# Kernel tuning notes

Measured on AMD Instinct MI355X. Metric: run time of the kernel, lower is better.

Reference implementation:

```python
import jax, jax.numpy as jnp
import numpy as np

N_NODES = 20000
N_EDGES = 640000
IN_NODE = 128
IN_EDGE = 16
HIDDEN = 64
OUT = 128
HEADS = 4
N_GRAPHS = 64
NEG_SLOPE = 0.2


def _glorot(key, shape):
    fan_in, fan_out = shape[0], shape[-1]
    s = jnp.sqrt(6.0 / (fan_in + fan_out)).astype(jnp.float32)
    return jax.random.uniform(key, shape, jnp.float32, -s, s)


def setup_inputs() -> dict:
    key = jax.random.key(0)
    ks = jax.random.split(key, 32)
    inp = {
        "x": jax.random.normal(ks[0], (N_NODES, IN_NODE), jnp.float32),
        "edge_attr": jax.random.normal(ks[1], (N_EDGES, IN_EDGE), jnp.float32),
        "edge_index": jax.random.randint(ks[2], (2, N_EDGES), 0, N_NODES),
        "batch": jnp.sort(jax.random.randint(ks[3], (N_NODES,), 0, N_GRAPHS)),
    }
    # layer dims: (in, out_per_head, concat)
    dims = [(IN_NODE, HIDDEN, True), (HIDDEN * HEADS, HIDDEN, True), (HIDDEN * HEADS, OUT, False)]
    k = 4
    for i, (cin, cout, concat) in enumerate(dims):
        hc = HEADS * cout
        inp[f"Wl{i}"] = _glorot(ks[k], (cin, hc)); k += 1
        inp[f"bl{i}"] = jnp.zeros((hc,), jnp.float32)
        inp[f"Wr{i}"] = _glorot(ks[k], (cin, hc)); k += 1
        inp[f"br{i}"] = jnp.zeros((hc,), jnp.float32)
        inp[f"We{i}"] = _glorot(ks[k], (IN_EDGE, hc)); k += 1
        inp[f"att{i}"] = _glorot(ks[k], (HEADS, cout)); k += 1
        inp[f"bias{i}"] = jnp.zeros((hc if concat else cout,), jnp.float32)
    return inp


def _gatv2_layer(x, edge_index, edge_attr, Wl, bl, Wr, br, We, att, bias, concat):
    """One PyG-style GATv2Conv layer with edge features."""
    H, C = att.shape
    N = x.shape[0]
    src, dst = edge_index[0], edge_index[1]
    xl = (x @ Wl + bl).reshape(N, H, C)  # messages from source
    xr = (x @ Wr + br).reshape(N, H, C)  # target query
    e = (edge_attr @ We).reshape(-1, H, C)
    m = jax.nn.leaky_relu(xl[src] + xr[dst] + e, NEG_SLOPE)  # [E,H,C]
    logits = jnp.einsum("ehc,hc->eh", m, att)  # [E,H]
    # scatter-softmax over edges grouped by destination node
    lmax = jax.ops.segment_max(logits, dst, num_segments=N)
    p = jnp.exp(logits - lmax[dst])
    denom = jax.ops.segment_sum(p, dst, num_segments=N)
    alpha = p / (denom[dst] + 1e-16)  # [E,H]
    out = jax.ops.segment_sum(alpha[:, :, None] * xl[src], dst, num_segments=N)  # [N,H,C]
    if concat:
        return out.reshape(N, H * C) + bias
    return out.mean(axis=1) + bias


def reference(x, edge_attr, edge_index, batch,
              Wl0, bl0, Wr0, br0, We0, att0, bias0,
              Wl1, bl1, Wr1, br1, We1, att1, bias1,
              Wl2, bl2, Wr2, br2, We2, att2, bias2):
    layers = [
        (Wl0, bl0, Wr0, br0, We0, att0, bias0, True),
        (Wl1, bl1, Wr1, br1, We1, att1, bias1, True),
        (Wl2, bl2, Wr2, br2, We2, att2, bias2, False),
    ]
    h = x
    for (Wl, bl, Wr, br, We, att, b, concat) in layers:
        h = _gatv2_layer(h, edge_index, edge_attr, Wl, bl, Wr, br, We, att, b, concat)
    # global max + mean pooling per graph
    x_max = jax.ops.segment_max(h, batch, num_segments=N_GRAPHS)
    s = jax.ops.segment_sum(h, batch, num_segments=N_GRAPHS)
    cnt = jax.ops.segment_sum(jnp.ones((h.shape[0], 1), h.dtype), batch, num_segments=N_GRAPHS)
    x_mean = s / jnp.maximum(cnt, 1.0)
    return jnp.concatenate([x_max, x_mean], axis=1)  # [G, 2*OUT]
```

## Files before the change

### kernel.cpp

```cpp
#include <hip/hip_runtime.h>

#define NB 8

typedef float f32x2 __attribute__((ext_vector_type(2)));

template <int K, int M>
__global__ __launch_bounds__(256) void node_gemm(
    const float* __restrict__ X, const float* __restrict__ W,
    const float* __restrict__ bias, float* __restrict__ Y) {
  constexpr int NPB = 16;
  constexpr int COLS4 = M / 4;
  constexpr int NG = 256 / COLS4;
  constexpr int RPN = NPB / NG;
  __shared__ float xs[NPB * K];
  const int tid = threadIdx.x;
  const int n0 = blockIdx.x * NPB;
  {
    const float4* X4 = reinterpret_cast<const float4*>(X + (size_t)n0 * K);
    float4* xs4 = reinterpret_cast<float4*>(xs);
    for (int i = tid; i < NPB * K / 4; i += 256) xs4[i] = X4[i];
  }
  __syncthreads();
  const int c4 = (tid % COLS4) * 4;
  const int r0 = (tid / COLS4) * RPN;
  float acc[RPN][4];
#pragma unroll
  for (int r = 0; r < RPN; ++r)
#pragma unroll
    for (int q = 0; q < 4; ++q) acc[r][q] = 0.f;

  for (int k = 0; k < K; k += 4) {
    float xv[RPN][4];
#pragma unroll
    for (int r = 0; r < RPN; ++r)
      *reinterpret_cast<float4*>(xv[r]) =
          *reinterpret_cast<const float4*>(&xs[(r0 + r) * K + k]);
#pragma unroll
    for (int j = 0; j < 4; ++j) {
      float wv[4];
      *reinterpret_cast<float4*>(wv) =
          *reinterpret_cast<const float4*>(&W[(size_t)(k + j) * M + c4]);
#pragma unroll
      for (int r = 0; r < RPN; ++r)
#pragma unroll
        for (int q = 0; q < 4; ++q)
          acc[r][q] = fmaf(xv[r][j], wv[q], acc[r][q]);
    }
  }
  float bv[4];
  *reinterpret_cast<float4*>(bv) = *reinterpret_cast<const float4*>(&bias[c4]);
#pragma unroll
  for (int r = 0; r < RPN; ++r) {
    float o[4];
#pragma unroll
    for (int q = 0; q < 4; ++q) o[q] = acc[r][q] + bv[q];
    *reinterpret_cast<float4*>(&Y[(size_t)(n0 + r0 + r) * M + c4]) =
        *reinterpret_cast<float4*>(o);
  }
}

__global__ void hist_b(const int* __restrict__ ei, int* __restrict__ kcnt,
                       int E, int bdiv) {
  int i = blockIdx.x * blockDim.x + threadIdx.x;
  if (i < E) atomicAdd(&kcnt[ei[E + i] * NB + ei[i] / bdiv], 1);
}

__global__ __launch_bounds__(1024) void blk_scan(
    const int* __restrict__ in, int* __restrict__ out1, int* __restrict__ bsum, int n) {
  __shared__ int buf[1024];
  const int tid = threadIdx.x;
  const int gid = blockIdx.x * 1024 + tid;
  int v = (gid < n) ? in[gid] : 0;
  buf[tid] = v;
  __syncthreads();
  for (int off = 1; off < 1024; off <<= 1) {
    int t = (tid >= off) ? buf[tid - off] : 0;
    __syncthreads();
    buf[tid] += t;
    __syncthreads();
  }
  if (gid < n) out1[gid] = buf[tid];
  if (tid == 1023) bsum[blockIdx.x] = buf[1023];
}

__global__ __launch_bounds__(256) void scan_bsum(int* __restrict__ bsum, int nb) {
  __shared__ int buf[256];
  const int tid = threadIdx.x;
  int v = (tid < nb) ? bsum[tid] : 0;
  buf[tid] = v;
  __syncthreads();
  for (int off = 1; off < 256; off <<= 1) {
    int t = (tid >= off) ? buf[tid - off] : 0;
    __syncthreads();
    buf[tid] += t;
    __syncthreads();
  }
  if (tid < nb) bsum[tid] = buf[tid];
}

__global__ void add_off(int* __restrict__ kptr, const int* __restrict__ bsum, int n) {
  int gid = blockIdx.x * blockDim.x + threadIdx.x;
  if (gid == 0) kptr[0] = 0;
  if (gid < n) {
    int blk = gid >> 10;
    if (blk > 0) kptr[1 + gid] += bsum[blk - 1];
  }
}

__global__ void csr_fill_b(const int* __restrict__ ei, const int* __restrict__ kptr,
                           int* __restrict__ kfill, int* __restrict__ csr_src,
                           int* __restrict__ csr_eid, int E, int bdiv) {
  int i = blockIdx.x * blockDim.x + threadIdx.x;
  if (i < E) {
    int src = ei[i], dst = ei[E + i];
    int key = dst * NB + src / bdiv;
    int slot = kptr[key] + atomicAdd(&kfill[key], 1);
    csr_src[slot] = src;
    csr_eid[slot] = i;
  }
}

__global__ void ea_perm(const float* __restrict__ ea, const int* __restrict__ csr_eid,
                        float* __restrict__ ea_csr, int E) {
  int i = blockIdx.x * blockDim.x + threadIdx.x;
  if (i < E * 16) {
    int slot = i >> 4;
    ea_csr[i] = ea[((size_t)csr_eid[slot] << 4) + (i & 15)];
  }
}

__global__ void graph_bounds(const int* __restrict__ batch, int* __restrict__ gstart,
                             int* __restrict__ gend, int N) {
  int i = blockIdx.x * blockDim.x + threadIdx.x;
  if (i < N) {
    int g = batch[i];
    atomicMin(&gstart[g], i);
    atomicMax(&gend[g], i + 1);
  }
}

template <int GS>
__device__ __forceinline__ void gat_edge_pk(
    const float4 a, const double (&c)[8], const float4 xrv,
    const f32x2 (&w01)[16], const f32x2 (&w23)[16], const float (&attv)[4],
    float& m, float& s, float (&acc)[4]) {
  f32x2 m01, m23;
  m01.x = a.x + xrv.x; m01.y = a.y + xrv.y;
  m23.x = a.z + xrv.z; m23.y = a.w + xrv.w;
#pragma unroll
  for (int i = 0; i < 8; ++i) {
    asm("v_pk_fma_f32 %0, %2, %3, %0 op_sel:[0,0,0] op_sel_hi:[0,1,1]\n\t"
        "v_pk_fma_f32 %1, %2, %4, %1 op_sel:[0,0,0] op_sel_hi:[0,1,1]\n\t"
        "v_pk_fma_f32 %0, %2, %5, %0 op_sel:[1,0,0] op_sel_hi:[1,1,1]\n\t"
        "v_pk_fma_f32 %1, %2, %6, %1 op_sel:[1,0,0] op_sel_hi:[1,1,1]"
        : "+v"(m01), "+v"(m23)
        : "s"(c[i]), "v"(w01[2 * i]), "v"(w23[2 * i]),
          "v"(w01[2 * i + 1]), "v"(w23[2 * i + 1]));
  }
  const float mv[4] = {m01.x, m01.y, m23.x, m23.y};
  float l = 0.f;
#pragma unroll
  for (int q = 0; q < 4; ++q) {
    const float v = fmaxf(mv[q], 0.2f * mv[q]);
    l = fmaf(v, attv[q], l);
  }
#pragma unroll
  for (int off = 1; off < GS; off <<= 1) l += __shfl_xor(l, off);
  const float nm = fmaxf(m, l);
  const float sc = __expf(m - nm);
  const float pe = __expf(l - nm);
  m = nm;
  s = fmaf(s, sc, pe);
  acc[0] = fmaf(pe, a.x, acc[0] * sc);
  acc[1] = fmaf(pe, a.y, acc[1] * sc);
  acc[2] = fmaf(pe, a.z, acc[2] * sc);
  acc[3] = fmaf(pe, a.w, acc[3] * sc);
}

template <int HCROW, int MODE>
__global__ __launch_bounds__(256) void fused_gat(
    const float* __restrict__ xl, const float* __restrict__ xr,
    const float* __restrict__ ea_csr, const float* __restrict__ We,
    const float* __restrict__ att, const float* __restrict__ bias,
    const int* __restrict__ kptr, const int* __restrict__ csr_src,
    float* __restrict__ out, float* __restrict__ outB, int N) {
  constexpr int C = HCROW / 4;
  constexpr int GS = C / 4;
  const int lane = threadIdx.x & 63;
  const int wslot = threadIdx.x >> 6;
  int bx = blockIdx.x;
  int colbase = 0;
  float* o_ptr = out;
  if (MODE == 1) {
    const int gb = gridDim.x >> 1;
    if (bx >= gb) { bx -= gb; colbase = 256; o_ptr = outB; }
  }
  const int dst = bx * 4 + wslot;
  if (dst >= N) return;

  f32x2 w01[16], w23[16];
#pragma unroll
  for (int k = 0; k < 16; ++k) {
    const float4 t =
        *reinterpret_cast<const float4*>(&We[k * HCROW + colbase + lane * 4]);
    w01[k].x = t.x; w01[k].y = t.y;
    w23[k].x = t.z; w23[k].y = t.w;
  }
  const int col0 = colbase + lane * 4;
  const int head = col0 / C;
  float attv[4];
  *reinterpret_cast<float4*>(attv) =
      *reinterpret_cast<const float4*>(&att[head * C + (col0 % C)]);
  const float4* xl4 = reinterpret_cast<const float4*>(xl);
  const int rs4 = HCROW / 4;
  const int coff = col0 >> 2;
  const float4 xrv =
      reinterpret_cast<const float4*>(xr)[(size_t)dst * rs4 + coff];
  const double* ed = reinterpret_cast<const double*>(ea_csr);

  const int row0 = __builtin_amdgcn_readfirstlane(kptr[dst * NB]);
  const int rend = __builtin_amdgcn_readfirstlane(kptr[dst * NB + NB]);

  float m = -__builtin_inff(), s = 0.f;
  float acc[4] = {0.f, 0.f, 0.f, 0.f};

  if (row0 < rend) {
    const int last = rend - 1;
    const int s0 = csr_src[row0];
    const int s1 = csr_src[min(row0 + 1, last)];
    const int s2 = csr_src[min(row0 + 2, last)];
    const int s3 = csr_src[min(row0 + 3, last)];
    float4 a0 = xl4[(size_t)s0 * rs4 + coff];
    float4 a1 = xl4[(size_t)s1 * rs4 + coff];
    float4 a2 = xl4[(size_t)s2 * rs4 + coff];
    float4 a3 = xl4[(size_t)s3 * rs4 + coff];
    int sr0 = csr_src[min(row0 + 4, last)];
    int sr1 = csr_src[min(row0 + 5, last)];
    double c0[8], c1[8];
    {
      const double* e0 = ed + (size_t)row0 * 8;
      const double* e1 = ed + (size_t)min(row0 + 1, last) * 8;
#pragma unroll
      for (int k = 0; k < 8; ++k) { c0[k] = e0[k]; c1[k] = e1[k]; }
    }

    for (int p = row0; p < rend; p += 2) {
      const float4 na0 = xl4[(size_t)sr0 * rs4 + coff];
      const float4 na1 = xl4[(size_t)sr1 * rs4 + coff];
      const int nsr0 = csr_src[min(p + 6, last)];
      const int nsr1 = csr_src[min(p + 7, last)];
      double cn0[8], cn1[8];
      {
        const double* e0 = ed + (size_t)min(p + 2, last) * 8;
        const double* e1 = ed + (size_t)min(p + 3, last) * 8;
#pragma unroll
        for (int k = 0; k < 8; ++k) { cn0[k] = e0[k]; cn1[k] = e1[k]; }
      }
      gat_edge_pk<GS>(a0, c0, xrv, w01, w23, attv, m, s, acc);
      if (p + 1 < rend) gat_edge_pk<GS>(a1, c1, xrv, w01, w23, attv, m, s, acc);
      a0 = a2; a1 = a3; a2 = na0; a3 = na1;
      sr0 = nsr0; sr1 = nsr1;
#pragma unroll
      for (int k = 0; k < 8; ++k) { c0[k] = cn0[k]; c1[k] = cn1[k]; }
    }
  }

  const float inv = 1.f / (s + 1e-16f);
  float o[4];
  if (MODE == 0) {
    float bv[4];
    *reinterpret_cast<float4*>(bv) = *reinterpret_cast<const float4*>(&bias[col0]);
#pragma unroll
    for (int q = 0; q < 4; ++q) o[q] = fmaf(acc[q], inv, bv[q]);
    *reinterpret_cast<float4*>(&o_ptr[(size_t)dst * HCROW + col0]) =
        *reinterpret_cast<float4*>(o);
  } else {
#pragma unroll
    for (int q = 0; q < 4; ++q) {
      o[q] = acc[q] * inv;
      o[q] += __shfl_xor(o[q], 32);
    }
    if (lane < 32)
      *reinterpret_cast<float4*>(&o_ptr[(size_t)dst * 128 + lane * 4]) =
          *reinterpret_cast<float4*>(o);
  }
}

__global__ __launch_bounds__(256) void pool_graph(
    const float* __restrict__ hA, const float* __restrict__ hB,
    const float* __restrict__ bias2, const int* __restrict__ gstart,
    const int* __restrict__ gend, float* __restrict__ out) {
  const int g = blockIdx.x;
  const int c = threadIdx.x & 127;
  const int sub = threadIdx.x >> 7;
  const int s0 = gstart[g], e0 = gend[g];
  const float b = bias2[c];
  float mx = -__builtin_inff(), sm = 0.f;
  for (int n = s0 + sub; n < e0; n += 2) {
    const float v = fmaf(0.25f, hA[(size_t)n * 128 + c] + hB[(size_t)n * 128 + c], b);
    mx = fmaxf(mx, v);
    sm += v;
  }
  __shared__ float smx[128], ssm[128];
  if (sub) { smx[c] = mx; ssm[c] = sm; }
  __syncthreads();
  if (!sub) {
    mx = fmaxf(mx, smx[c]);
    sm += ssm[c];
    const int cnt = e0 - s0;
    out[g * 256 + c] = (cnt > 0) ? mx : 0.f;
    out[g * 256 + 128 + c] = sm / fmaxf((float)cnt, 1.f);
  }
}

extern "C" void kernel_launch(void* const* d_in, const int* in_sizes, int n_in,
                              void* d_out, int out_size, void* d_ws, size_t ws_size,
                              hipStream_t stream) {
  const float* x     = (const float*)d_in[0];
  const float* ea    = (const float*)d_in[1];
  const int*   ei    = (const int*)d_in[2];
  const int*   batch = (const int*)d_in[3];
  const int N = in_sizes[0] / 128;
  const int E = in_sizes[2] / 2;
  const int NBINS = N * NB;
  const int bdiv = (N + NB - 1) / NB;

  const float* Wl[3]   = {(const float*)d_in[4],  (const float*)d_in[11], (const float*)d_in[18]};
  const float* blv[3]  = {(const float*)d_in[5],  (const float*)d_in[12], (const float*)d_in[19]};
  const float* Wr[3]   = {(const float*)d_in[6],  (const float*)d_in[13], (const float*)d_in[20]};
  const float* brv[3]  = {(const float*)d_in[7],  (const float*)d_in[14], (const float*)d_in[21]};
  const float* Wev[3]  = {(const float*)d_in[8],  (const float*)d_in[15], (const float*)d_in[22]};
  const float* attv[3] = {(const float*)d_in[9],  (const float*)d_in[16], (const float*)d_in[23]};
  const float* bias[3] = {(const float*)d_in[10], (const float*)d_in[17], (const float*)d_in[24]};

  float* ws = (float*)d_ws;
  float* xl     = ws;
  float* xr     = xl + (size_t)N * 512;
  float* ea_csr = xr + (size_t)N * 512;
  float* h      = ea_csr + (size_t)E * 16;
  int* kptr     = (int*)(h + (size_t)N * 256);
  int* csr_src  = kptr + (NBINS + 1);
  int* bsum     = csr_src + E;
  int* gstart   = bsum + 257;
  int* gend     = gstart + 64;
  int* csr_eid = (int*)h;
  int* kcnt    = csr_eid + E;
  int* kfill   = kcnt + NBINS;
  float* hsumA = h;
  float* hsumB = h + (size_t)N * 128;
  (void)n_in; (void)out_size; (void)ws_size;

  const int nodeBlocks = N / 16;
  const int edgeBlocks = (E + 255) / 256;
  const int scanBlocks = (NBINS + 1023) / 1024;
  const int gatBlocks = (N + 3) / 4;

  hipMemsetAsync(kcnt, 0, (size_t)2 * NBINS * sizeof(int), stream);
  hipMemsetAsync(gstart, 0x7f, 64 * sizeof(int), stream);
  hipMemsetAsync(gend, 0, 64 * sizeof(int), stream);
  hist_b<<<edgeBlocks, 256, 0, stream>>>(ei, kcnt, E, bdiv);
  graph_bounds<<<(N + 255) / 256, 256, 0, stream>>>(batch, gstart, gend, N);
  blk_scan<<<scanBlocks, 1024, 0, stream>>>(kcnt, kptr + 1, bsum, NBINS);
  scan_bsum<<<1, 256, 0, stream>>>(bsum, scanBlocks);
  add_off<<<(NBINS + 255) / 256, 256, 0, stream>>>(kptr, bsum, NBINS);
  csr_fill_b<<<edgeBlocks, 256, 0, stream>>>(ei, kptr, kfill, csr_src, csr_eid, E, bdiv);
  ea_perm<<<(E * 16 + 255) / 256, 256, 0, stream>>>(ea, csr_eid, ea_csr, E);

  node_gemm<128, 256><<<nodeBlocks, 256, 0, stream>>>(x, Wl[0], blv[0], xl);
  node_gemm<128, 256><<<nodeBlocks, 256, 0, stream>>>(x, Wr[0], brv[0], xr);
  fused_gat<256, 0><<<gatBlocks, 256, 0, stream>>>(
      xl, xr, ea_csr, Wev[0], attv[0], bias[0], kptr, csr_src, h, nullptr, N);

  node_gemm<256, 256><<<nodeBlocks, 256, 0, stream>>>(h, Wl[1], blv[1], xl);
  node_gemm<256, 256><<<nodeBlocks, 256, 0, stream>>>(h, Wr[1], brv[1], xr);
  fused_gat<256, 0><<<gatBlocks, 256, 0, stream>>>(
      xl, xr, ea_csr, Wev[1], attv[1], bias[1], kptr, csr_src, h, nullptr, N);

  node_gemm<256, 512><<<nodeBlocks, 256, 0, stream>>>(h, Wl[2], blv[2], xl);
  node_gemm<256, 512><<<nodeBlocks, 256, 0, stream>>>(h, Wr[2], brv[2], xr);
  fused_gat<512, 1><<<2 * gatBlocks, 256, 0, stream>>>(
      xl, xr, ea_csr, Wev[2], attv[2], bias[2], kptr, csr_src, hsumA, hsumB, N);

  pool_graph<<<64, 256, 0, stream>>>(hsumA, hsumB, bias[2], gstart, gend, (float*)d_out);
}
```

Baseline: 1.112 ms.

## Merge paired node GEMMs, deepen gather prefetch, interleave head halves, refine bins

Each pair of Wl/Wr node GEMMs becomes one launch that picks weights by block index, removing a launch and the gap between them. The fused GAT kernel now prefetches eight source rows ahead instead of four, giving more loads in flight to hide gather latency at the cost of extra registers. The last layer now interleaves its two column halves across adjacent blocks so both halves of a destination node run close together and share cache. The CSR bin factor NB rises from 8 to 32, so the block-sum scan grows to 1024 threads and the workspace offsets are adjusted to match.

```diff
diff --git a/kernel.cpp b/kernel.cpp
--- a/kernel.cpp
+++ b/kernel.cpp
@@ -1,20 +1,26 @@
 #include <hip/hip_runtime.h>
 
-#define NB 8
+#define NB 32
 
 typedef float f32x2 __attribute__((ext_vector_type(2)));
 
 template <int K, int M>
-__global__ __launch_bounds__(256) void node_gemm(
-    const float* __restrict__ X, const float* __restrict__ W,
-    const float* __restrict__ bias, float* __restrict__ Y) {
+__global__ __launch_bounds__(256) void node_gemm2(
+    const float* __restrict__ X, const float* __restrict__ W1,
+    const float* __restrict__ b1, float* __restrict__ Y1,
+    const float* __restrict__ W2, const float* __restrict__ b2,
+    float* __restrict__ Y2, int nodeBlocks) {
   constexpr int NPB = 16;
   constexpr int COLS4 = M / 4;
   constexpr int NG = 256 / COLS4;
   constexpr int RPN = NPB / NG;
   __shared__ float xs[NPB * K];
   const int tid = threadIdx.x;
-  const int n0 = blockIdx.x * NPB;
+  const int hi = blockIdx.x >= nodeBlocks;
+  const float* W = hi ? W2 : W1;
+  const float* bias = hi ? b2 : b1;
+  float* Y = hi ? Y2 : Y1;
+  const int n0 = (hi ? blockIdx.x - nodeBlocks : blockIdx.x) * NPB;
   {
     const float4* X4 = reinterpret_cast<const float4*>(X + (size_t)n0 * K);
     float4* xs4 = reinterpret_cast<float4*>(xs);
@@ -83,13 +89,13 @@
   if (tid == 1023) bsum[blockIdx.x] = buf[1023];
 }
 
-__global__ __launch_bounds__(256) void scan_bsum(int* __restrict__ bsum, int nb) {
-  __shared__ int buf[256];
+__global__ __launch_bounds__(1024) void scan_bsum(int* __restrict__ bsum, int nb) {
+  __shared__ int buf[1024];
   const int tid = threadIdx.x;
   int v = (tid < nb) ? bsum[tid] : 0;
   buf[tid] = v;
   __syncthreads();
-  for (int off = 1; off < 256; off <<= 1) {
+  for (int off = 1; off < 1024; off <<= 1) {
     int t = (tid >= off) ? buf[tid - off] : 0;
     __syncthreads();
     buf[tid] += t;
@@ -192,8 +198,9 @@
   int colbase = 0;
   float* o_ptr = out;
   if (MODE == 1) {
-    const int gb = gridDim.x >> 1;
-    if (bx >= gb) { bx -= gb; colbase = 256; o_ptr = outB; }
+    colbase = (bx & 1) * 256;
+    if (bx & 1) o_ptr = outB;
+    bx >>= 1;
   }
   const int dst = bx * 4 + wslot;
   if (dst >= N) return;
@@ -226,16 +233,19 @@
 
   if (row0 < rend) {
     const int last = rend - 1;
-    const int s0 = csr_src[row0];
-    const int s1 = csr_src[min(row0 + 1, last)];
-    const int s2 = csr_src[min(row0 + 2, last)];
-    const int s3 = csr_src[min(row0 + 3, last)];
-    float4 a0 = xl4[(size_t)s0 * rs4 + coff];
-    float4 a1 = xl4[(size_t)s1 * rs4 + coff];
-    float4 a2 = xl4[(size_t)s2 * rs4 + coff];
-    float4 a3 = xl4[(size_t)s3 * rs4 + coff];
-    int sr0 = csr_src[min(row0 + 4, last)];
-    int sr1 = csr_src[min(row0 + 5, last)];
+    int sp[8];
+#pragma unroll
+    for (int i = 0; i < 8; ++i) sp[i] = csr_src[min(row0 + i, last)];
+    float4 a0 = xl4[(size_t)sp[0] * rs4 + coff];
+    float4 a1 = xl4[(size_t)sp[1] * rs4 + coff];
+    float4 a2 = xl4[(size_t)sp[2] * rs4 + coff];
+    float4 a3 = xl4[(size_t)sp[3] * rs4 + coff];
+    float4 a4 = xl4[(size_t)sp[4] * rs4 + coff];
+    float4 a5 = xl4[(size_t)sp[5] * rs4 + coff];
+    float4 a6 = xl4[(size_t)sp[6] * rs4 + coff];
+    float4 a7 = xl4[(size_t)sp[7] * rs4 + coff];
+    int sr0 = csr_src[min(row0 + 8, last)];
+    int sr1 = csr_src[min(row0 + 9, last)];
     double c0[8], c1[8];
     {
       const double* e0 = ed + (size_t)row0 * 8;
@@ -247,8 +257,8 @@
     for (int p = row0; p < rend; p += 2) {
       const float4 na0 = xl4[(size_t)sr0 * rs4 + coff];
       const float4 na1 = xl4[(size_t)sr1 * rs4 + coff];
-      const int nsr0 = csr_src[min(p + 6, last)];
-      const int nsr1 = csr_src[min(p + 7, last)];
+      const int nsr0 = csr_src[min(p + 10, last)];
+      const int nsr1 = csr_src[min(p + 11, last)];
       double cn0[8], cn1[8];
       {
         const double* e0 = ed + (size_t)min(p + 2, last) * 8;
@@ -258,7 +268,7 @@
       }
       gat_edge_pk<GS>(a0, c0, xrv, w01, w23, attv, m, s, acc);
       if (p + 1 < rend) gat_edge_pk<GS>(a1, c1, xrv, w01, w23, attv, m, s, acc);
-      a0 = a2; a1 = a3; a2 = na0; a3 = na1;
+      a0 = a2; a1 = a3; a2 = a4; a3 = a5; a4 = a6; a5 = a7; a6 = na0; a7 = na1;
       sr0 = nsr0; sr1 = nsr1;
 #pragma unroll
       for (int k = 0; k < 8; ++k) { c0[k] = cn0[k]; c1[k] = cn1[k]; }
@@ -341,7 +351,7 @@
   int* kptr     = (int*)(h + (size_t)N * 256);
   int* csr_src  = kptr + (NBINS + 1);
   int* bsum     = csr_src + E;
-  int* gstart   = bsum + 257;
+  int* gstart   = bsum + 1024;
   int* gend     = gstart + 64;
   int* csr_eid = (int*)h;
   int* kcnt    = csr_eid + E;
@@ -361,23 +371,23 @@
   hist_b<<<edgeBlocks, 256, 0, stream>>>(ei, kcnt, E, bdiv);
   graph_bounds<<<(N + 255) / 256, 256, 0, stream>>>(batch, gstart, gend, N);
   blk_scan<<<scanBlocks, 1024, 0, stream>>>(kcnt, kptr + 1, bsum, NBINS);
-  scan_bsum<<<1, 256, 0, stream>>>(bsum, scanBlocks);
+  scan_bsum<<<1, 1024, 0, stream>>>(bsum, scanBlocks);
   add_off<<<(NBINS + 255) / 256, 256, 0, stream>>>(kptr, bsum, NBINS);
   csr_fill_b<<<edgeBlocks, 256, 0, stream>>>(ei, kptr, kfill, csr_src, csr_eid, E, bdiv);
   ea_perm<<<(E * 16 + 255) / 256, 256, 0, stream>>>(ea, csr_eid, ea_csr, E);
 
-  node_gemm<128, 256><<<nodeBlocks, 256, 0, stream>>>(x, Wl[0], blv[0], xl);
-  node_gemm<128, 256><<<nodeBlocks, 256, 0, stream>>>(x, Wr[0], brv[0], xr);
+  node_gemm2<128, 256><<<2 * nodeBlocks, 256, 0, stream>>>(
+      x, Wl[0], blv[0], xl, Wr[0], brv[0], xr, nodeBlocks);
   fused_gat<256, 0><<<gatBlocks, 256, 0, stream>>>(
       xl, xr, ea_csr, Wev[0], attv[0], bias[0], kptr, csr_src, h, nullptr, N);
 
-  node_gemm<256, 256><<<nodeBlocks, 256, 0, stream>>>(h, Wl[1], blv[1], xl);
-  node_gemm<256, 256><<<nodeBlocks, 256, 0, stream>>>(h, Wr[1], brv[1], xr);
+  node_gemm2<256, 256><<<2 * nodeBlocks, 256, 0, stream>>>(
+      h, Wl[1], blv[1], xl, Wr[1], brv[1], xr, nodeBlocks);
   fused_gat<256, 0><<<gatBlocks, 256, 0, stream>>>(
       xl, xr, ea_csr, Wev[1], attv[1], bias[1], kptr, csr_src, h, nullptr, N);
 
-  node_gemm<256, 512><<<nodeBlocks, 256, 0, stream>>>(h, Wl[2], blv[2], xl);
-  node_gemm<256, 512><<<nodeBlocks, 256, 0, stream>>>(h, Wr[2], brv[2], xr);
+  node_gemm2<256, 512><<<2 * nodeBlocks, 256, 0, stream>>>(
+      h, Wl[2], blv[2], xl, Wr[2], brv[2], xr, nodeBlocks);
   fused_gat<512, 1><<<2 * gatBlocks, 256, 0, stream>>>(
       xl, xr, ea_csr, Wev[2], attv[2], bias[2], kptr, csr_src, hsumA, hsumB, N);
 
```

Measured after the change: 1.200 ms. 1.08x slower.
